# Kernel optimization log

Hardware: AMD Instinct MI355X
Metric: run time of the kernel (lower is better)

## Reference

```python
import jax, jax.numpy as jnp
import numpy as np

B, T, D = 2, 2048, 1024
N_HEADS = 16
HEAD_DIM = D // N_HEADS


def setup_inputs() -> dict:
    key = jax.random.key(0)
    ks = jax.random.split(key, 5)
    s = 0.02
    return {
        "x": jax.random.normal(ks[0], (B, T, D), jnp.float32),
        "wq": jax.random.normal(ks[1], (D, D), jnp.float32) * s,
        "wk": jax.random.normal(ks[2], (D, D), jnp.float32) * s,
        "wv": jax.random.normal(ks[3], (D, D), jnp.float32) * s,
        "wo": jax.random.normal(ks[4], (D, D), jnp.float32) * s,
        "bo": jnp.zeros((D,), jnp.float32),
    }


def reference(x, wq, wk, wv, wo, bo):
    b, t, _ = x.shape
    # QKV projections (weights stored [d_in, d_out]); reshape to (b, heads, t, head_dim)
    def split_heads(y):
        return y.reshape(b, t, N_HEADS, HEAD_DIM).transpose(0, 2, 1, 3)
    q = split_heads(x @ wq)
    k = split_heads(x @ wk)
    v = split_heads(x @ wv)
    # causal attention scores: (b, h, t, t)
    scores = jnp.einsum("bhqd,bhkd->bhqk", q, k)
    causal = jnp.tril(jnp.ones((t, t), bool))  # True where attending allowed
    scores = jnp.where(causal, scores, -jnp.inf)
    attn = jax.nn.softmax(scores / np.sqrt(HEAD_DIM).astype(np.float32), axis=-1)
    # dropout_rate = 0.0 (eval mode) -> identity
    ctx = jnp.einsum("bhqk,bhkd->bhqd", attn, v)
    ctx = ctx.transpose(0, 2, 1, 3).reshape(b, t, D)
    return ctx @ wo + bo
```

## Files before the change

### kernel.cpp

```cpp
#include <hip/hip_runtime.h>
#include <hip/hip_bf16.h>
#include <cstdint>

typedef __hip_bfloat16 bf16;
typedef __bf16 bf16x8 __attribute__((ext_vector_type(8)));
typedef __bf16 bf16x4 __attribute__((ext_vector_type(4)));
typedef float f32x4 __attribute__((ext_vector_type(4)));
typedef uint32_t u32x4 __attribute__((ext_vector_type(4)));

#define LOG2E 1.4426950408889634f

__device__ __forceinline__ void gload_lds16(const void* g, void* l) {
  __builtin_amdgcn_global_load_lds(
      (const __attribute__((address_space(1))) unsigned int*)g,
      (__attribute__((address_space(3))) unsigned int*)l,
      16, 0, 0);
}

__device__ __forceinline__ uint32_t pack_bf16(float a, float b) {
  const uint32_t ha = (uint32_t)__builtin_bit_cast(uint16_t, (__bf16)a);
  const uint32_t hb = (uint32_t)__builtin_bit_cast(uint16_t, (__bf16)b);
  return ha | (hb << 16);
}

__global__ __launch_bounds__(256) void prep(
    const float* __restrict__ x, bf16* __restrict__ xb,
    const float* __restrict__ wq, const float* __restrict__ wk,
    const float* __restrict__ wv, const float* __restrict__ wo,
    bf16* __restrict__ dqkv, bf16* __restrict__ dout) {
  __shared__ float tile[32][33];
  const int bid = blockIdx.x;
  if (bid < 2048) {
    const int i = (bid * 256 + threadIdx.x) * 8;
    const f32x4 a = *(const f32x4*)(x + i);
    const f32x4 b = *(const f32x4*)(x + i + 4);
    bf16x8 o;
#pragma unroll
    for (int j = 0; j < 4; ++j) { o[j] = (__bf16)a[j]; o[4 + j] = (__bf16)b[j]; }
    *(bf16x8*)(xb + i) = o;
    return;
  }
  const int id = bid - 2048;
  const int z = id >> 10;
  const int t2 = id & 1023;
  const int bx = (t2 & 31) * 32, by = (t2 >> 5) * 32;
  const int tx = threadIdx.x & 31, ty = threadIdx.x >> 5;
  const float* src = (z == 0) ? wq : ((z == 1) ? wk : ((z == 2) ? wv : wo));
  bf16* dst = (z < 3) ? (dqkv + (long)z * 1048576) : dout;
  for (int j = ty; j < 32; j += 8)
    tile[j][tx] = src[(long)(by + j) * 1024 + bx + tx];
  __syncthreads();
  for (int j = ty; j < 32; j += 8)
    dst[(long)(bx + j) * 1024 + by + tx] = __float2bfloat16(tile[tx][j]);
}

__global__ __launch_bounds__(256, 3) void gemm_qkv(
    const bf16* __restrict__ A, const bf16* __restrict__ Bt,
    bf16* __restrict__ Cq, bf16* __restrict__ Ck, bf16* __restrict__ Cv,
    int M, int N, int K) {
  __shared__ __align__(16) bf16 As[128 * 64];
  __shared__ __align__(16) bf16 Bs[96 * 64];

  const int tid = threadIdx.x;
  const int lane = tid & 63;
  const int wave = tid >> 6;
  const int quad = lane >> 4;
  const int l16 = lane & 15;
  const int id = (int)blockIdx.y * 32 + (int)blockIdx.x;
  const int xcd = id & 7, idx = id >> 3;
  const int bxn = xcd * 4 + (idx & 3);
  const int byn = idx >> 2;
  const int m0 = byn * 128;
  const int n0 = bxn * 96;
  const int wm = (wave >> 1) * 64;
  const int wn = (wave & 1) * 48;

  const f32x4 zero4 = {0.f, 0.f, 0.f, 0.f};
  f32x4 acc[4][3];
#pragma unroll
  for (int mi = 0; mi < 4; ++mi)
#pragma unroll
    for (int ni = 0; ni < 3; ++ni) acc[mi][ni] = zero4;

  const int sRow = tid >> 3;
  const int sK = (tid & 7) * 8;
  const int sSwz = sK ^ (8 * (sRow & 7));
  const bf16* Ag = A + (long)(m0 + sRow) * K + sSwz;
  const bf16* Bg = Bt + (long)(n0 + sRow) * K + sSwz;
  const int swzr = 8 * (l16 & 7);

  for (int k0 = 0; k0 < K; k0 += 64) {
#pragma unroll
    for (int j = 0; j < 4; ++j)
      gload_lds16(Ag + k0 + (long)(32 * j) * K, &As[tid * 8 + 2048 * j]);
#pragma unroll
    for (int j = 0; j < 3; ++j)
      gload_lds16(Bg + k0 + (long)(32 * j) * K, &Bs[tid * 8 + 2048 * j]);
    __syncthreads();

#pragma unroll
    for (int ks = 0; ks < 64; ks += 32) {
      const int colr = (ks + quad * 8) ^ swzr;
      bf16x8 af[4], bfv[3];
#pragma unroll
      for (int mi = 0; mi < 4; ++mi)
        af[mi] = *(const bf16x8*)&As[(wm + mi * 16 + l16) * 64 + colr];
#pragma unroll
      for (int ni = 0; ni < 3; ++ni)
        bfv[ni] = *(const bf16x8*)&Bs[(wn + ni * 16 + l16) * 64 + colr];
#pragma unroll
      for (int mi = 0; mi < 4; ++mi)
#pragma unroll
        for (int ni = 0; ni < 3; ++ni)
          acc[mi][ni] = __builtin_amdgcn_mfma_f32_16x16x32_bf16(af[mi], bfv[ni], acc[mi][ni], 0, 0, 0);
    }
    __syncthreads();
  }

#pragma unroll
  for (int mi = 0; mi < 4; ++mi) {
    const int gmb = m0 + wm + mi * 16 + quad * 4;
#pragma unroll
    for (int ni = 0; ni < 3; ++ni) {
      const int n = n0 + wn + ni * 16 + l16;
      const int which = n >> 10, rem = n & 1023;
      const int h = rem >> 6, hd = rem & 63;
      bf16* dst = (which == 0) ? Cq : ((which == 1) ? Ck : Cv);
#pragma unroll
      for (int r = 0; r < 4; ++r) {
        const int gm = gmb + r;
        const int b = gm >> 11, t = gm & 2047;
        dst[(((long)(b * 16 + h)) * 2048 + t) * 64 + hd] = __float2bfloat16(acc[mi][ni][r]);
      }
    }
  }
}

__global__ __launch_bounds__(256, 3) void gemm_out(
    const bf16* __restrict__ A, const bf16* __restrict__ Bt,
    const float* __restrict__ bias, float* __restrict__ Cout,
    int M, int N, int K) {
  __shared__ __align__(16) bf16 As[64 * 64];
  __shared__ __align__(16) bf16 Bs[128 * 64];

  const int tid = threadIdx.x;
  const int lane = tid & 63;
  const int wave = tid >> 6;
  const int quad = lane >> 4;
  const int l16 = lane & 15;
  const int id = (int)blockIdx.y * 8 + (int)blockIdx.x;
  const int m0 = (id >> 3) * 64;
  const int n0 = (id & 7) * 128;
  const int wm = (wave & 1) * 32;
  const int wn = (wave >> 1) * 64;

  const f32x4 zero4 = {0.f, 0.f, 0.f, 0.f};
  f32x4 acc[2][4];
#pragma unroll
  for (int mi = 0; mi < 2; ++mi)
#pragma unroll
    for (int ni = 0; ni < 4; ++ni) acc[mi][ni] = zero4;

  const int sRow = tid >> 3;
  const int sK = (tid & 7) * 8;
  const int sSwz = sK ^ (8 * (sRow & 7));
  const bf16* Ag = A + (long)(m0 + sRow) * K + sSwz;
  const bf16* Bg = Bt + (long)(n0 + sRow) * K + sSwz;
  const int swzr = 8 * (l16 & 7);

  for (int k0 = 0; k0 < K; k0 += 64) {
#pragma unroll
    for (int j = 0; j < 2; ++j)
      gload_lds16(Ag + k0 + (long)(32 * j) * K, &As[tid * 8 + 2048 * j]);
#pragma unroll
    for (int j = 0; j < 4; ++j)
      gload_lds16(Bg + k0 + (long)(32 * j) * K, &Bs[tid * 8 + 2048 * j]);
    __syncthreads();

#pragma unroll
    for (int ks = 0; ks < 64; ks += 32) {
      const int colr = (ks + quad * 8) ^ swzr;
      bf16x8 af[2], bfv[4];
#pragma unroll
      for (int mi = 0; mi < 2; ++mi)
        af[mi] = *(const bf16x8*)&As[(wm + mi * 16 + l16) * 64 + colr];
#pragma unroll
      for (int ni = 0; ni < 4; ++ni)
        bfv[ni] = *(const bf16x8*)&Bs[(wn + ni * 16 + l16) * 64 + colr];
#pragma unroll
      for (int mi = 0; mi < 2; ++mi)
#pragma unroll
        for (int ni = 0; ni < 4; ++ni)
          acc[mi][ni] = __builtin_amdgcn_mfma_f32_16x16x32_bf16(af[mi], bfv[ni], acc[mi][ni], 0, 0, 0);
    }
    __syncthreads();
  }

#pragma unroll
  for (int mi = 0; mi < 2; ++mi) {
    const int gmb = m0 + wm + mi * 16 + quad * 4;
#pragma unroll
    for (int ni = 0; ni < 4; ++ni) {
      const int n = n0 + wn + ni * 16 + l16;
      const float bv = bias[n];
#pragma unroll
      for (int r = 0; r < 4; ++r)
        Cout[(long)(gmb + r) * N + n] = acc[mi][ni][r] + bv;
    }
  }
}

__global__ __launch_bounds__(256, 3) void attn_kernel(
    const bf16* __restrict__ Q, const bf16* __restrict__ Kg, const bf16* __restrict__ Vg,
    bf16* __restrict__ ctx) {
  constexpr int KSTR = 72, VSTR = 136;
  __shared__ __align__(16) bf16 Ks[128 * KSTR];
  __shared__ __align__(16) bf16 Vt[64 * VSTR];

  const int tid = threadIdx.x;
  const int lane = tid & 63;
  const int wave = tid >> 6;
  const int quad = lane >> 4;
  const int l16 = lane & 15;

  const int id = (int)blockIdx.y * 16 + (int)blockIdx.x;
  const int g = id & 7;
  const int bh = g * 4 + ((id >> 3) & 3);
  const int p = id >> 5;

  const long base = (long)bh * 2048 * 64;
  const int b = bh >> 4, h = bh & 15;

  const int krow = tid >> 1;
  const int kc32 = (tid & 1) * 32;
  const int vr4 = (tid & 31) * 4;
  const int vd8 = (tid >> 5) * 8;
  const int vb4 = (vr4 >> 4) & 1;
  const int vc4 = (vr4 & ~31) + 8 * (((vr4 >> 2) & 3) ^ vb4) + 4 * vb4;

  const float negsh = -12.0f * LOG2E;
  const f32x4 zero4 = {0.f, 0.f, 0.f, 0.f};

#pragma unroll 1
  for (int seg = 0; seg < 2; ++seg) {
    const int qt = seg ? (31 - p) : p;
    const int qbase = qt * 64 + wave * 16;
    const int q = qbase + l16;

    bf16x8 qf0 = *(const bf16x8*)(Q + base + (long)(qbase + l16) * 64 + quad * 8);
    bf16x8 qf1 = *(const bf16x8*)(Q + base + (long)(qbase + l16) * 64 + 32 + quad * 8);
#pragma unroll
    for (int j = 0; j < 8; ++j) {
      qf0[j] = (__bf16)((float)qf0[j] * 0.125f);
      qf1[j] = (__bf16)((float)qf1[j] * 0.125f);
    }

    float l_part = 0.f;
    f32x4 oacc[4];
#pragma unroll
    for (int nb = 0; nb < 4; ++nb) oacc[nb] = zero4;

    const int nk = (qt + 2) >> 1;
    bf16x8 kr[4], vv[4];
    {
      const bf16* kp = Kg + base + (long)krow * 64 + kc32;
#pragma unroll
      for (int i = 0; i < 4; ++i) kr[i] = *(const bf16x8*)(kp + i * 8);
#pragma unroll
      for (int i = 0; i < 4; ++i)
        vv[i] = *(const bf16x8*)(Vg + base + (long)(vr4 + i) * 64 + vd8);
    }

    for (int kt = 0; kt < nk; ++kt) {
      const int k0 = kt * 128;
#pragma unroll
      for (int i = 0; i < 4; ++i)
        *(bf16x8*)&Ks[krow * KSTR + kc32 + i * 8] = kr[i];
#pragma unroll
      for (int j = 0; j < 8; ++j) {
        bf16x4 t;
        t[0] = vv[0][j]; t[1] = vv[1][j]; t[2] = vv[2][j]; t[3] = vv[3][j];
        *(bf16x4*)&Vt[(vd8 + j) * VSTR + vc4] = t;
      }
      __syncthreads();
      if (kt + 1 < nk) {
        const bf16* kp = Kg + base + (long)(k0 + 128 + krow) * 64 + kc32;
#pragma unroll
        for (int i = 0; i < 4; ++i) kr[i] = *(const bf16x8*)(kp + i * 8);
#pragma unroll
        for (int i = 0; i < 4; ++i)
          vv[i] = *(const bf16x8*)(Vg + base + (long)(k0 + 128 + vr4 + i) * 64 + vd8);
      }

      f32x4 s8[8];
      __builtin_amdgcn_s_setprio(1);
#pragma unroll
      for (int kb = 0; kb < 8; ++kb) {
        const bf16x8 kb0 = *(const bf16x8*)&Ks[(kb * 16 + l16) * KSTR + quad * 8];
        const bf16x8 kb1 = *(const bf16x8*)&Ks[(kb * 16 + l16) * KSTR + 32 + quad * 8];
        f32x4 a = zero4;
        a = __builtin_amdgcn_mfma_f32_16x16x32_bf16(kb0, qf0, a, 0, 0, 0);
        a = __builtin_amdgcn_mfma_f32_16x16x32_bf16(kb1, qf1, a, 0, 0, 0);
        s8[kb] = a;
      }
      __builtin_amdgcn_s_setprio(0);

      if (kt == nk - 1) {
        const int qg = q - k0 - quad * 4;
#pragma unroll
        for (int kb = 0; kb < 8; ++kb)
#pragma unroll
          for (int r = 0; r < 4; ++r)
            s8[kb][r] = (kb * 16 + r <= qg) ? s8[kb][r] : -1e30f;
      }

      float rsum = 0.f;
      u32x4 paw[4];
#pragma unroll
      for (int kk = 0; kk < 4; ++kk) {
        const float p0 = exp2f(fmaf(s8[2 * kk][0], LOG2E, negsh));
        const float p1 = exp2f(fmaf(s8[2 * kk][1], LOG2E, negsh));
        const float p2 = exp2f(fmaf(s8[2 * kk][2], LOG2E, negsh));
        const float p3 = exp2f(fmaf(s8[2 * kk][3], LOG2E, negsh));
        const float p4 = exp2f(fmaf(s8[2 * kk + 1][0], LOG2E, negsh));
        const float p5 = exp2f(fmaf(s8[2 * kk + 1][1], LOG2E, negsh));
        const float p6 = exp2f(fmaf(s8[2 * kk + 1][2], LOG2E, negsh));
        const float p7 = exp2f(fmaf(s8[2 * kk + 1][3], LOG2E, negsh));
        rsum += ((p0 + p1) + (p2 + p3)) + ((p4 + p5) + (p6 + p7));
        u32x4 w;
        w[0] = pack_bf16(p0, p1);
        w[1] = pack_bf16(p2, p3);
        w[2] = (uint32_t)__shfl_xor((int)pack_bf16(p4, p5), 16);
        w[3] = (uint32_t)__shfl_xor((int)pack_bf16(p6, p7), 16);
        paw[kk] = w;
      }
      l_part += rsum;

      __builtin_amdgcn_s_setprio(1);
#pragma unroll
      for (int kk = 0; kk < 4; ++kk) {
        const bf16x8 pa = __builtin_bit_cast(bf16x8, paw[kk]);
#pragma unroll
        for (int nb2 = 0; nb2 < 4; ++nb2) {
          const bf16x8 vb = *(const bf16x8*)&Vt[(nb2 * 16 + l16) * VSTR + kk * 32 + quad * 8];
          oacc[nb2] = __builtin_amdgcn_mfma_f32_16x16x32_bf16(pa, vb, oacc[nb2], 0, 0, 0);
        }
      }
      __builtin_amdgcn_s_setprio(0);
      __syncthreads();
    }

    float l_i = l_part;
    l_i += __shfl_xor(l_i, 16);
    l_i += __shfl_xor(l_i, 32);

    float linv[4];
#pragma unroll
    for (int r = 0; r < 4; ++r) linv[r] = 1.0f / __shfl(l_i, quad * 4 + r);
#pragma unroll
    for (int r = 0; r < 4; ++r) {
      const int t = qbase + quad * 4 + r;
#pragma unroll
      for (int nb2 = 0; nb2 < 4; ++nb2) {
        const int d = h * 64 + nb2 * 16 + l16;
        ctx[((long)b * 2048 + t) * 1024 + d] = __float2bfloat16(oacc[nb2][r] * linv[r]);
      }
    }
  }
}

extern "C" void kernel_launch(void* const* d_in, const int* in_sizes, int n_in,
                              void* d_out, int out_size, void* d_ws, size_t ws_size,
                              hipStream_t stream) {
  const float* x  = (const float*)d_in[0];
  const float* wq = (const float*)d_in[1];
  const float* wk = (const float*)d_in[2];
  const float* wv = (const float*)d_in[3];
  const float* wo = (const float*)d_in[4];
  const float* bo = (const float*)d_in[5];
  float* out = (float*)d_out;

  bf16* Wtqkv = (bf16*)d_ws;
  bf16* Wto   = Wtqkv + 3145728;
  bf16* xb    = Wto + 1048576;
  bf16* Qb    = xb + 4194304;
  bf16* Kb    = Qb + 4194304;
  bf16* Vb    = Kb + 4194304;
  bf16* Cx    = xb;

  hipLaunchKernelGGL(prep, dim3(6144), dim3(256), 0, stream,
                     x, xb, wq, wk, wv, wo, Wtqkv, Wto);

  hipLaunchKernelGGL(gemm_qkv, dim3(32, 32), dim3(256), 0, stream,
                     xb, Wtqkv, Qb, Kb, Vb, 4096, 3072, 1024);

  hipLaunchKernelGGL(attn_kernel, dim3(16, 32), dim3(256), 0, stream, Qb, Kb, Vb, Cx);

  hipLaunchKernelGGL(gemm_out, dim3(8, 64), dim3(256), 0, stream,
                     Cx, Wto, bo, out, 4096, 1024, 1024);
}
```

Before: 178.0 us.

## Double-buffer K via direct global-to-LDS loads and skip masked tail blocks

K tiles now load straight into a double-buffered, XOR-swizzled LDS array through global_load_lds, so they no longer pass through registers and the next tile's load overlaps compute. The last (diagonal) key tile is peeled into its own block that skips the QK, exp and PV work for 16-key sub-blocks lying entirely above the causal diagonal for each wave. This trades more LDS (two K buffers) for fewer registers and less wasted work, which may affect occupancy at 3 blocks per CU.

```diff
diff --git a/kernel.cpp b/kernel.cpp
--- a/kernel.cpp
+++ b/kernel.cpp
@@ -213,8 +213,8 @@
 __global__ __launch_bounds__(256, 3) void attn_kernel(
     const bf16* __restrict__ Q, const bf16* __restrict__ Kg, const bf16* __restrict__ Vg,
     bf16* __restrict__ ctx) {
-  constexpr int KSTR = 72, VSTR = 136;
-  __shared__ __align__(16) bf16 Ks[128 * KSTR];
+  constexpr int VSTR = 136;
+  __shared__ __align__(16) bf16 Ks2[2][128 * 64];
   __shared__ __align__(16) bf16 Vt[64 * VSTR];
 
   const int tid = threadIdx.x;
@@ -231,8 +231,10 @@
   const long base = (long)bh * 2048 * 64;
   const int b = bh >> 4, h = bh & 15;
 
-  const int krow = tid >> 1;
-  const int kc32 = (tid & 1) * 32;
+  const int sRowK = tid >> 3;
+  const int sSwzK = ((tid & 7) * 8) ^ (8 * (sRowK & 7));
+  const int kswz = 8 * (l16 & 7);
+
   const int vr4 = (tid & 31) * 4;
   const int vd8 = (tid >> 5) * 8;
   const int vb4 = (vr4 >> 4) & 1;
@@ -261,21 +263,21 @@
     for (int nb = 0; nb < 4; ++nb) oacc[nb] = zero4;
 
     const int nk = (qt + 2) >> 1;
-    bf16x8 kr[4], vv[4];
+    int cur = 0;
+
     {
-      const bf16* kp = Kg + base + (long)krow * 64 + kc32;
-#pragma unroll
-      for (int i = 0; i < 4; ++i) kr[i] = *(const bf16x8*)(kp + i * 8);
-#pragma unroll
-      for (int i = 0; i < 4; ++i)
-        vv[i] = *(const bf16x8*)(Vg + base + (long)(vr4 + i) * 64 + vd8);
-    }
-
-    for (int kt = 0; kt < nk; ++kt) {
+      const bf16* kp = Kg + base + (long)sRowK * 64 + sSwzK;
+#pragma unroll
+      for (int j = 0; j < 4; ++j)
+        gload_lds16(kp + (long)(32 * j) * 64, &Ks2[0][tid * 8 + 2048 * j]);
+    }
+    bf16x8 vv[4];
+#pragma unroll
+    for (int i = 0; i < 4; ++i)
+      vv[i] = *(const bf16x8*)(Vg + base + (long)(vr4 + i) * 64 + vd8);
+
+    for (int kt = 0; kt < nk - 1; ++kt) {
       const int k0 = kt * 128;
-#pragma unroll
-      for (int i = 0; i < 4; ++i)
-        *(bf16x8*)&Ks[krow * KSTR + kc32 + i * 8] = kr[i];
 #pragma unroll
       for (int j = 0; j < 8; ++j) {
         bf16x4 t;
@@ -283,36 +285,30 @@
         *(bf16x4*)&Vt[(vd8 + j) * VSTR + vc4] = t;
       }
       __syncthreads();
-      if (kt + 1 < nk) {
-        const bf16* kp = Kg + base + (long)(k0 + 128 + krow) * 64 + kc32;
-#pragma unroll
-        for (int i = 0; i < 4; ++i) kr[i] = *(const bf16x8*)(kp + i * 8);
-#pragma unroll
-        for (int i = 0; i < 4; ++i)
-          vv[i] = *(const bf16x8*)(Vg + base + (long)(k0 + 128 + vr4 + i) * 64 + vd8);
-      }
-
+
+      {
+        const bf16* kp = Kg + base + (long)(k0 + 128 + sRowK) * 64 + sSwzK;
+#pragma unroll
+        for (int j = 0; j < 4; ++j)
+          gload_lds16(kp + (long)(32 * j) * 64, &Ks2[cur ^ 1][tid * 8 + 2048 * j]);
+      }
+#pragma unroll
+      for (int i = 0; i < 4; ++i)
+        vv[i] = *(const bf16x8*)(Vg + base + (long)(k0 + 128 + vr4 + i) * 64 + vd8);
+
+      const bf16* ksc = &Ks2[cur][0];
       f32x4 s8[8];
       __builtin_amdgcn_s_setprio(1);
 #pragma unroll
       for (int kb = 0; kb < 8; ++kb) {
-        const bf16x8 kb0 = *(const bf16x8*)&Ks[(kb * 16 + l16) * KSTR + quad * 8];
-        const bf16x8 kb1 = *(const bf16x8*)&Ks[(kb * 16 + l16) * KSTR + 32 + quad * 8];
+        const bf16x8 kb0 = *(const bf16x8*)&ksc[(kb * 16 + l16) * 64 + ((quad * 8) ^ kswz)];
+        const bf16x8 kb1 = *(const bf16x8*)&ksc[(kb * 16 + l16) * 64 + ((32 + quad * 8) ^ kswz)];
         f32x4 a = zero4;
         a = __builtin_amdgcn_mfma_f32_16x16x32_bf16(kb0, qf0, a, 0, 0, 0);
         a = __builtin_amdgcn_mfma_f32_16x16x32_bf16(kb1, qf1, a, 0, 0, 0);
         s8[kb] = a;
       }
       __builtin_amdgcn_s_setprio(0);
-
-      if (kt == nk - 1) {
-        const int qg = q - k0 - quad * 4;
-#pragma unroll
-        for (int kb = 0; kb < 8; ++kb)
-#pragma unroll
-          for (int r = 0; r < 4; ++r)
-            s8[kb][r] = (kb * 16 + r <= qg) ? s8[kb][r] : -1e30f;
-      }
 
       float rsum = 0.f;
       u32x4 paw[4];
@@ -348,6 +344,84 @@
       }
       __builtin_amdgcn_s_setprio(0);
       __syncthreads();
+      cur ^= 1;
+    }
+
+    {
+      const int k0 = (nk - 1) * 128;
+#pragma unroll
+      for (int j = 0; j < 8; ++j) {
+        bf16x4 t;
+        t[0] = vv[0][j]; t[1] = vv[1][j]; t[2] = vv[2][j]; t[3] = vv[3][j];
+        *(bf16x4*)&Vt[(vd8 + j) * VSTR + vc4] = t;
+      }
+      __syncthreads();
+
+      const int nkb = ((qbase + 15 - k0) >> 4) + 1;
+      int kbLim = (nkb + 1) & ~1;
+      if (kbLim > 8) kbLim = 8;
+      const int kkLim = kbLim >> 1;
+
+      const bf16* ksc = &Ks2[cur][0];
+      f32x4 s8[8];
+      __builtin_amdgcn_s_setprio(1);
+#pragma unroll
+      for (int kb = 0; kb < 8; ++kb)
+        if (kb < kbLim) {
+          const bf16x8 kb0 = *(const bf16x8*)&ksc[(kb * 16 + l16) * 64 + ((quad * 8) ^ kswz)];
+          const bf16x8 kb1 = *(const bf16x8*)&ksc[(kb * 16 + l16) * 64 + ((32 + quad * 8) ^ kswz)];
+          f32x4 a = zero4;
+          a = __builtin_amdgcn_mfma_f32_16x16x32_bf16(kb0, qf0, a, 0, 0, 0);
+          a = __builtin_amdgcn_mfma_f32_16x16x32_bf16(kb1, qf1, a, 0, 0, 0);
+          s8[kb] = a;
+        }
+      __builtin_amdgcn_s_setprio(0);
+
+      const int qg = q - k0 - quad * 4;
+#pragma unroll
+      for (int kb = 0; kb < 8; ++kb)
+        if (kb < kbLim) {
+#pragma unroll
+          for (int r = 0; r < 4; ++r)
+            s8[kb][r] = (kb * 16 + r <= qg) ? s8[kb][r] : -1e30f;
+        }
+
+      float rsum = 0.f;
+      u32x4 paw[4];
+#pragma unroll
+      for (int kk = 0; kk < 4; ++kk)
+        if (kk < kkLim) {
+          const float p0 = exp2f(fmaf(s8[2 * kk][0], LOG2E, negsh));
+          const float p1 = exp2f(fmaf(s8[2 * kk][1], LOG2E, negsh));
+          const float p2 = exp2f(fmaf(s8[2 * kk][2], LOG2E, negsh));
+          const float p3 = exp2f(fmaf(s8[2 * kk][3], LOG2E, negsh));
+          const float p4 = exp2f(fmaf(s8[2 * kk + 1][0], LOG2E, negsh));
+          const float p5 = exp2f(fmaf(s8[2 * kk + 1][1], LOG2E, negsh));
+          const float p6 = exp2f(fmaf(s8[2 * kk + 1][2], LOG2E, negsh));
+          const float p7 = exp2f(fmaf(s8[2 * kk + 1][3], LOG2E, negsh));
+          rsum += ((p0 + p1) + (p2 + p3)) + ((p4 + p5) + (p6 + p7));
+          u32x4 w;
+          w[0] = pack_bf16(p0, p1);
+          w[1] = pack_bf16(p2, p3);
+          w[2] = (uint32_t)__shfl_xor((int)pack_bf16(p4, p5), 16);
+          w[3] = (uint32_t)__shfl_xor((int)pack_bf16(p6, p7), 16);
+          paw[kk] = w;
+        }
+      l_part += rsum;
+
+      __builtin_amdgcn_s_setprio(1);
+#pragma unroll
+      for (int kk = 0; kk < 4; ++kk)
+        if (kk < kkLim) {
+          const bf16x8 pa = __builtin_bit_cast(bf16x8, paw[kk]);
+#pragma unroll
+          for (int nb2 = 0; nb2 < 4; ++nb2) {
+            const bf16x8 vb = *(const bf16x8*)&Vt[(nb2 * 16 + l16) * VSTR + kk * 32 + quad * 8];
+            oacc[nb2] = __builtin_amdgcn_mfma_f32_16x16x32_bf16(pa, vb, oacc[nb2], 0, 0, 0);
+          }
+        }
+      __builtin_amdgcn_s_setprio(0);
+      __syncthreads();
     }
 
     float l_i = l_part;
```

New measurement: 191.0 us. 7.3% more time.
